# Performance work log

Measured on AMD Instinct MI355X. Metric: run time of the kernel, lower is better.

The kernel has to match this reference:

```python
import jax, jax.numpy as jnp
import numpy as np

B, N = 16, 4096
N_IN, E_OUT = 128, 128          # inpt_dim[1], outp_dim[0]
OUT_N = 128                     # outp_dim[1]
G_DIM, CTXT_DIM = 64, 64
NODE_IN = E_OUT + N_IN          # 256, pre_ln size
CTXT_IN = G_DIM + CTXT_DIM      # 128
HID_F, HID_A = 256, 128
N_HEADS = 4
HEAD_DIM = OUT_N // N_HEADS     # 32
LN_EPS = 1e-5


def _init_w(key, fan_in, fan_out):
    return jax.random.normal(key, (fan_in, fan_out), jnp.float32) / np.float32(np.sqrt(fan_in))


def setup_inputs() -> dict:
    key = jax.random.key(0)
    ks = jax.random.split(key, 10)
    nodes = jax.random.normal(ks[0], (B, N, N_IN), jnp.float32)
    pooled_edges = jax.random.normal(ks[1], (B, N, E_OUT), jnp.float32)
    # variable-length graphs: valid prefix per graph (at least half the nodes)
    lengths = jax.random.randint(ks[2], (B,), N // 2, N + 1)
    mask = jnp.arange(N)[None, :] < lengths[:, None]
    globs = jax.random.normal(ks[3], (B, G_DIM), jnp.float32)
    ctxt = jax.random.normal(ks[4], (B, CTXT_DIM), jnp.float32)
    return {
        "nodes": nodes,
        "pooled_edges": pooled_edges,
        "mask": mask,
        "globs": globs,
        "ctxt": ctxt,
        "ln_g": jnp.ones((NODE_IN,), jnp.float32),
        "ln_b": jnp.zeros((NODE_IN,), jnp.float32),
        "feat_w1": _init_w(ks[5], NODE_IN + CTXT_IN, HID_F),
        "feat_b1": jnp.zeros((HID_F,), jnp.float32),
        "feat_w2": _init_w(ks[6], HID_F, OUT_N),
        "feat_b2": jnp.zeros((OUT_N,), jnp.float32),
        "attn_w1": _init_w(ks[7], NODE_IN + CTXT_IN, HID_A),
        "attn_b1": jnp.zeros((HID_A,), jnp.float32),
        "attn_w2": _init_w(ks[8], HID_A, N_HEADS),
        "attn_b2": jnp.zeros((N_HEADS,), jnp.float32),
    }


def _mlp(x, w1, b1, w2, b2):
    # DenseNetwork: one hidden block with LeakyReLU ("lrlu"), linear output
    h = jax.nn.leaky_relu(x @ w1 + b1)
    return h @ w2 + b2


def reference(nodes, pooled_edges, mask, globs, ctxt, ln_g, ln_b,
              feat_w1, feat_b1, feat_w2, feat_b2,
              attn_w1, attn_b1, attn_w2, attn_b2):
    # nodes = cat([graph.nodes, pooled_edges]) -> pre-LayerNorm
    x = jnp.concatenate([nodes, pooled_edges], axis=-1)           # [B,N,256]
    mu = jnp.mean(x, axis=-1, keepdims=True)
    var = jnp.var(x, axis=-1, keepdims=True)
    x = (x - mu) * jax.lax.rsqrt(var + LN_EPS) * ln_g + ln_b

    # high-level context broadcast to every node
    hl = jnp.concatenate([globs, ctxt], axis=-1)                   # [B,128]
    hl = jnp.broadcast_to(hl[:, None, :], (x.shape[0], x.shape[1], hl.shape[-1]))
    xin = jnp.concatenate([x, hl], axis=-1)                        # [B,N,384]

    # attention net with -inf padding, softmax over node axis (dim=-2)
    logits = _mlp(xin, attn_w1, attn_b1, attn_w2, attn_b2)          # [B,N,H]
    logits = jnp.where(mask[..., None], logits, -jnp.inf)
    w = jax.nn.softmax(logits, axis=1) / np.float32(np.sqrt(OUT_N))
    w = jnp.where(mask[..., None], w, 0.0)

    # feature net with 0 padding + residual (same_size)
    feats = _mlp(xin, feat_w1, feat_b1, feat_w2, feat_b2)           # [B,N,128]
    feats = jnp.where(mask[..., None], feats, 0.0)
    new_nodes = feats + nodes

    # expand per-head weights across head_dim, flatten, weighted node pooling
    w_full = jnp.repeat(w, HEAD_DIM, axis=-1)                       # [B,N,128]
    pooled = jnp.sum(new_nodes * w_full, axis=1)                    # [B,128]
    return (new_nodes, pooled)
```

## Files before the change

### kernel.cpp

```cpp
#include <hip/hip_runtime.h>
#include <stdint.h>

typedef unsigned short u16;
typedef unsigned char  u8;
typedef unsigned int   u32;
typedef __attribute__((ext_vector_type(8))) short bf16x8;
typedef __attribute__((ext_vector_type(4))) float f32x4;

static __device__ __forceinline__ float bf2f(u32 u) {
    union { u32 i; float f; } x; x.i = u << 16; return x.f;
}
static __device__ __forceinline__ u16 f2bf(float f) {
    union { u32 i; float f; } x; x.f = f;
    return (u16)((x.i + 0x7fffu + ((x.i >> 16) & 1u)) >> 16);
}
static __device__ __forceinline__ u32 packbf(float a, float b) {
    return (u32)f2bf(a) | ((u32)f2bf(b) << 16);
}
static __device__ __forceinline__ float ldf(const void* p, int i, int isf32) {
    return isf32 ? ((const float*)p)[i] : bf2f(((const u16*)p)[i]);
}
static __device__ __forceinline__ bool mvalid(const void* mask, int g, int mi32) {
    return mi32 ? (((const int*)mask)[g] != 0) : (((const u8*)mask)[g] != 0);
}

#define NTOT 65536
#define SXLD 260
#define SHLD 132
#define PVLD 136

__global__ __launch_bounds__(256) void k0_prep(
    const void* __restrict__ feat_w1, const void* __restrict__ attn_w1,
    const void* __restrict__ feat_b1, const void* __restrict__ attn_b1,
    const void* __restrict__ feat_w2, const void* __restrict__ attn_w2,
    const void* __restrict__ globs, const void* __restrict__ ctxt,
    const void* __restrict__ ln_g,
    u16* __restrict__ W1t, u16* __restrict__ W2t, u16* __restrict__ aw2t,
    float* __restrict__ hlc)
{
    __shared__ u16 tile[64][66];
    __shared__ float hl[128];
    const int isf32 = (((const u32*)ln_g)[0] == 0x3F800000u);
    const int bid = blockIdx.x;
    const int t = threadIdx.x;

    if (bid < 24) {
        int jt = bid >> 2, kt = bid & 3;
        int j0 = jt * 64, k0 = kt * 64;
        int jj = t & 63, kq = t >> 6;
#pragma unroll
        for (int r = 0; r < 16; r++) {
            int kk = r * 4 + kq;
            int j = j0 + jj;
            float v = (j < 256) ? ldf(feat_w1, (k0 + kk) * 256 + j, isf32)
                                : ldf(attn_w1, (k0 + kk) * 128 + (j - 256), isf32);
            tile[kk][jj] = f2bf(v);
        }
        __syncthreads();
        int kk2 = t & 63, jq = t >> 6;
#pragma unroll
        for (int r = 0; r < 16; r++) {
            int jj2 = r * 4 + jq;
            W1t[(size_t)(j0 + jj2) * 256 + k0 + kk2] = tile[kk2][jj2];
        }
    } else if (bid < 32) {
        int id2 = bid - 24;
        int ct2 = id2 >> 2, kt = id2 & 3;
        int c0 = ct2 * 64, k0 = kt * 64;
        int cc = t & 63, kq = t >> 6;
#pragma unroll
        for (int r = 0; r < 16; r++) {
            int kk = r * 4 + kq;
            tile[kk][cc] = f2bf(ldf(feat_w2, (k0 + kk) * 128 + c0 + cc, isf32));
        }
        __syncthreads();
        int kk2 = t & 63, cq = t >> 6;
#pragma unroll
        for (int r = 0; r < 16; r++) {
            int cc2 = r * 4 + cq;
            W2t[(size_t)(c0 + cc2) * 256 + k0 + kk2] = tile[kk2][cc2];
        }
    } else if (bid == 32) {
#pragma unroll
        for (int i = 0; i < 8; i++) {
            int e = i * 256 + t;
            int n = e >> 7, k = e & 127;
            aw2t[e] = (n < 4) ? f2bf(ldf(attn_w2, k * 4 + n, isf32)) : (u16)0;
        }
    } else {
        int b = bid - 33;
        if (t < 64)       hl[t] = ldf(globs, b * 64 + t, isf32);
        else if (t < 128) hl[t] = ldf(ctxt, b * 64 + (t - 64), isf32);
        __syncthreads();
        {
            float s = ldf(feat_b1, t, isf32);
#pragma unroll 8
            for (int c = 0; c < 128; c++)
                s += hl[c] * ldf(feat_w1, (256 + c) * 256 + t, isf32);
            hlc[b * 384 + t] = s;
        }
        if (t < 128) {
            float s = ldf(attn_b1, t, isf32);
#pragma unroll 8
            for (int c = 0; c < 128; c++)
                s += hl[c] * ldf(attn_w1, (256 + c) * 128 + t, isf32);
            hlc[b * 384 + 256 + t] = s;
        }
    }
}

__global__ __launch_bounds__(256, 3) void k_mega(
    const void* __restrict__ nodes, const void* __restrict__ edges,
    const void* __restrict__ ln_g, const void* __restrict__ ln_b,
    const u16* __restrict__ W1t, const u16* __restrict__ W2t,
    const u16* __restrict__ aw2t, const float* __restrict__ hlc,
    const void* __restrict__ attn_b2, const void* __restrict__ feat_b2,
    const void* __restrict__ mask,
    float* __restrict__ pv, void* __restrict__ outp)
{
    __shared__ __align__(16) u16 sX[64 * SXLD];
    __shared__ __align__(16) u16 sH[64 * SHLD];
    __shared__ float sG[256], sBt[256];
    __shared__ float sL[64][4];
    const int t = threadIdx.x;
    const int g0 = blockIdx.x * 64;
    const int b = g0 >> 12;
    const int isf32 = (((const u32*)ln_g)[0] == 0x3F800000u);
    const int mi32  = (((const u32*)mask)[0] == 1u);

    sG[t]  = ldf(ln_g, t, isf32);
    sBt[t] = ldf(ln_b, t, isf32);
    __syncthreads();

#pragma unroll
    for (int half = 0; half < 2; half++) {
        const int r = half * 32 + (t >> 3), q8 = t & 7;
        u32 pk[16];
#pragma unroll
        for (int j = 0; j < 4; j++) {
            int c = q8 + j * 8;
            if (isf32) {
                const float* src = (c < 16)
                    ? ((const float*)nodes + (size_t)(g0 + r) * 128 + c * 8)
                    : ((const float*)edges + (size_t)(g0 + r) * 128 + (c - 16) * 8);
                float4 v0 = ((const float4*)src)[0];
                float4 v1 = ((const float4*)src)[1];
                pk[4 * j]     = packbf(v0.x, v0.y);
                pk[4 * j + 1] = packbf(v0.z, v0.w);
                pk[4 * j + 2] = packbf(v1.x, v1.y);
                pk[4 * j + 3] = packbf(v1.z, v1.w);
            } else {
                const u16* src = (c < 16)
                    ? ((const u16*)nodes + (size_t)(g0 + r) * 128 + c * 8)
                    : ((const u16*)edges + (size_t)(g0 + r) * 128 + (c - 16) * 8);
                uint4 v = ((const uint4*)src)[0];
                pk[4 * j] = v.x; pk[4 * j + 1] = v.y;
                pk[4 * j + 2] = v.z; pk[4 * j + 3] = v.w;
            }
        }
        float s = 0.f, q = 0.f;
#pragma unroll
        for (int i = 0; i < 16; i++) {
            float lo = bf2f(pk[i] & 0xffffu), hi = bf2f(pk[i] >> 16);
            s += lo + hi; q += lo * lo + hi * hi;
        }
        s += __shfl_xor(s, 1, 64); s += __shfl_xor(s, 2, 64); s += __shfl_xor(s, 4, 64);
        q += __shfl_xor(q, 1, 64); q += __shfl_xor(q, 2, 64); q += __shfl_xor(q, 4, 64);
        float mu = s * (1.f / 256.f);
        float var = q * (1.f / 256.f) - mu * mu;
        float rs = rsqrtf(var + 1e-5f);
#pragma unroll
        for (int j = 0; j < 4; j++) {
            int c = q8 + j * 8;
            u32 ow[4];
#pragma unroll
            for (int k2 = 0; k2 < 4; k2++) {
                int col = c * 8 + k2 * 2;
                u32 w2 = pk[4 * j + k2];
                float y0 = (bf2f(w2 & 0xffffu) - mu) * rs * sG[col]     + sBt[col];
                float y1 = (bf2f(w2 >> 16)     - mu) * rs * sG[col + 1] + sBt[col + 1];
                ow[k2] = packbf(y0, y1);
            }
            *(uint4*)&sX[r * SXLD + c * 8] = make_uint4(ow[0], ow[1], ow[2], ow[3]);
        }
    }
    __syncthreads();

    const int w = t >> 6, l = t & 63;
    const int lr = l & 15, lq = l >> 4;
    const float ab2 = (lr < 4) ? ldf(attn_b2, lr, isf32) : 0.f;
    const float fb2_0 = ldf(feat_b2, w * 32 + lr, isf32);
    const float fb2_1 = ldf(feat_b2, w * 32 + 16 + lr, isf32);

    f32x4 acc2[4][2];
#pragma unroll
    for (int rt = 0; rt < 4; rt++)
#pragma unroll
        for (int ct = 0; ct < 2; ct++) acc2[rt][ct] = (f32x4){0.f, 0.f, 0.f, 0.f};

    const int order[3] = {2, 0, 1};
#pragma unroll
    for (int oi = 0; oi < 3; oi++) {
        const int nt = order[oi];

        float hbv[2];
#pragma unroll
        for (int ct = 0; ct < 2; ct++)
            hbv[ct] = hlc[b * 384 + nt * 128 + w * 32 + ct * 16 + lr];

        f32x4 acc1[4][2];
#pragma unroll
        for (int rt = 0; rt < 4; rt++)
#pragma unroll
            for (int ct = 0; ct < 2; ct++) acc1[rt][ct] = (f32x4){0.f, 0.f, 0.f, 0.f};

        const u16* Wp = W1t + (size_t)(nt * 128 + w * 32 + lr) * 256;
#pragma unroll
        for (int kh = 0; kh < 2; kh++) {
            bf16x8 bW[4][2];
#pragma unroll
            for (int kk = 0; kk < 4; kk++)
#pragma unroll
                for (int ct = 0; ct < 2; ct++)
                    bW[kk][ct] = *(const bf16x8*)(Wp + ct * 16 * 256 + (kh * 4 + kk) * 32 + lq * 8);
#pragma unroll
            for (int kk = 0; kk < 4; kk++) {
                bf16x8 aF[4];
#pragma unroll
                for (int rt = 0; rt < 4; rt++)
                    aF[rt] = *(const bf16x8*)&sX[(rt * 16 + lr) * SXLD + ((kh * 4 + kk) * 4 + lq) * 8];
#pragma unroll
                for (int rt = 0; rt < 4; rt++)
#pragma unroll
                    for (int ct = 0; ct < 2; ct++)
                        acc1[rt][ct] = __builtin_amdgcn_mfma_f32_16x16x32_bf16(aF[rt], bW[kk][ct], acc1[rt][ct], 0, 0, 0);
            }
        }

        __syncthreads();
#pragma unroll
        for (int rt = 0; rt < 4; rt++)
#pragma unroll
            for (int ct = 0; ct < 2; ct++)
#pragma unroll
                for (int reg = 0; reg < 4; reg++) {
                    int row = rt * 16 + lq * 4 + reg;
                    int col = w * 32 + ct * 16 + lr;
                    float hv = acc1[rt][ct][reg] + hbv[ct];
                    hv = (hv >= 0.f) ? hv : 0.01f * hv;
                    sH[row * SHLD + col] = f2bf(hv);
                }
        __syncthreads();

        if (nt == 2) {
            f32x4 accL = (f32x4){0.f, 0.f, 0.f, 0.f};
#pragma unroll
            for (int kk = 0; kk < 4; kk++) {
                bf16x8 aF = *(const bf16x8*)&sH[(w * 16 + lr) * SHLD + (kk * 4 + lq) * 8];
                bf16x8 bF = *(const bf16x8*)(aw2t + lr * 128 + kk * 32 + lq * 8);
                accL = __builtin_amdgcn_mfma_f32_16x16x32_bf16(aF, bF, accL, 0, 0, 0);
            }
            if (lr < 4) {
#pragma unroll
                for (int reg = 0; reg < 4; reg++)
                    sL[w * 16 + lq * 4 + reg][lr] = accL[reg] + ab2;
            }
        } else {
            const u16* W2p = W2t + (size_t)(w * 32 + lr) * 256 + nt * 128;
            bf16x8 bW2[4][2];
#pragma unroll
            for (int kk = 0; kk < 4; kk++)
#pragma unroll
                for (int ct = 0; ct < 2; ct++)
                    bW2[kk][ct] = *(const bf16x8*)(W2p + ct * 16 * 256 + kk * 32 + lq * 8);
#pragma unroll
            for (int kk = 0; kk < 4; kk++) {
                bf16x8 aF[4];
#pragma unroll
                for (int rt = 0; rt < 4; rt++)
                    aF[rt] = *(const bf16x8*)&sH[(rt * 16 + lr) * SHLD + (kk * 4 + lq) * 8];
#pragma unroll
                for (int rt = 0; rt < 4; rt++)
#pragma unroll
                    for (int ct = 0; ct < 2; ct++)
                        acc2[rt][ct] = __builtin_amdgcn_mfma_f32_16x16x32_bf16(aF[rt], bW2[kk][ct], acc2[rt][ct], 0, 0, 0);
            }
        }
    }

    float* pvb = pv + (size_t)blockIdx.x * PVLD;
    if (w == 0) {
        const int row = l;
        const bool vld = mvalid(mask, g0 + row, mi32);
        float lg0 = sL[row][0], lg1 = sL[row][1], lg2 = sL[row][2], lg3 = sL[row][3];
        float x0 = vld ? lg0 : -1e30f;
        float x1 = vld ? lg1 : -1e30f;
        float x2 = vld ? lg2 : -1e30f;
        float x3 = vld ? lg3 : -1e30f;
#pragma unroll
        for (int o = 1; o < 64; o <<= 1) {
            x0 = fmaxf(x0, __shfl_xor(x0, o, 64));
            x1 = fmaxf(x1, __shfl_xor(x1, o, 64));
            x2 = fmaxf(x2, __shfl_xor(x2, o, 64));
            x3 = fmaxf(x3, __shfl_xor(x3, o, 64));
        }
        float e0 = vld ? expf(lg0 - x0) : 0.f;
        float e1 = vld ? expf(lg1 - x1) : 0.f;
        float e2 = vld ? expf(lg2 - x2) : 0.f;
        float e3 = vld ? expf(lg3 - x3) : 0.f;
        sL[row][0] = e0; sL[row][1] = e1; sL[row][2] = e2; sL[row][3] = e3;
        float s0 = e0, s1 = e1, s2 = e2, s3 = e3;
#pragma unroll
        for (int o = 1; o < 64; o <<= 1) {
            s0 += __shfl_xor(s0, o, 64);
            s1 += __shfl_xor(s1, o, 64);
            s2 += __shfl_xor(s2, o, 64);
            s3 += __shfl_xor(s3, o, 64);
        }
        if (l == 0) {
            pvb[128] = s0; pvb[129] = s1; pvb[130] = s2; pvb[131] = s3;
            pvb[132] = x0; pvb[133] = x1; pvb[134] = x2; pvb[135] = x3;
        }
    }
    __syncthreads();

    float pc0 = 0.f, pc1 = 0.f;
#pragma unroll
    for (int rt = 0; rt < 4; rt++)
#pragma unroll
        for (int ct = 0; ct < 2; ct++)
#pragma unroll
            for (int reg = 0; reg < 4; reg++) {
                int row = rt * 16 + lq * 4 + reg;
                int col = w * 32 + ct * 16 + lr;
                int g = g0 + row;
                float v = acc2[rt][ct][reg] + (ct ? fb2_1 : fb2_0);
                v = mvalid(mask, g, mi32) ? v : 0.f;
                v += ldf(nodes, g * 128 + col, isf32);
                size_t idx = (size_t)g * 128 + col;
                if (isf32) ((float*)outp)[idx] = v;
                else       ((u16*)outp)[idx] = f2bf(v);
                float e = sL[row][w];
                if (ct) pc1 += e * v; else pc0 += e * v;
            }
    pc0 += __shfl_xor(pc0, 16, 64); pc0 += __shfl_xor(pc0, 32, 64);
    pc1 += __shfl_xor(pc1, 16, 64); pc1 += __shfl_xor(pc1, 32, 64);
    if (lq == 0) {
        pvb[w * 32 + lr]      = pc0;
        pvb[w * 32 + 16 + lr] = pc1;
    }
}

__global__ __launch_bounds__(256) void k_final(
    const float* __restrict__ pv, const void* __restrict__ ln_g,
    void* __restrict__ outbase)
{
    __shared__ float sm[64][4], ss[64][4], se[64][4];
    __shared__ float sZ[4];
    __shared__ float part[2][128];
    const int b = blockIdx.x;
    const int t = threadIdx.x;
    const int isf32 = (((const u32*)ln_g)[0] == 0x3F800000u);
    const float* pvb = pv + (size_t)b * 64 * PVLD;

#pragma unroll
    for (int i = t; i < 512; i += 256) {
        int rec = i >> 3, j = i & 7;
        float x = pvb[(size_t)rec * PVLD + 128 + j];
        if (j < 4) ss[rec][j] = x;
        else       sm[rec][j - 4] = x;
    }
    __syncthreads();

    {
        const int h = t >> 6, i = t & 63;
        float m = sm[i][h];
#pragma unroll
        for (int o = 1; o < 64; o <<= 1) m = fmaxf(m, __shfl_xor(m, o, 64));
        float e = expf(sm[i][h] - m);
        se[i][h] = e;
        float z = e * ss[i][h];
#pragma unroll
        for (int o = 1; o < 64; o <<= 1) z += __shfl_xor(z, o, 64);
        if (i == 0) sZ[h] = z;
    }
    __syncthreads();

    {
        const int c = t & 127, half = t >> 7;
        const int h = c >> 5;
        float acc = 0.f;
#pragma unroll 8
        for (int j = 0; j < 32; j++) {
            int rec = half * 32 + j;
            acc += se[rec][h] * pvb[(size_t)rec * PVLD + c];
        }
        part[half][c] = acc;
    }
    __syncthreads();
    if (t < 128) {
        float p = (part[0][t] + part[1][t]) * (0.08838834764831845f / sZ[t >> 5]);
        size_t off = (size_t)NTOT * 128 + (size_t)b * 128 + t;
        if (isf32) ((float*)outbase)[off] = p;
        else       ((u16*)outbase)[off] = f2bf(p);
    }
}

extern "C" void kernel_launch(void* const* d_in, const int* in_sizes, int n_in,
                              void* d_out, int out_size, void* d_ws, size_t ws_size,
                              hipStream_t stream)
{
    const void* nodes   = d_in[0];
    const void* edges   = d_in[1];
    const void* mask    = d_in[2];
    const void* globs   = d_in[3];
    const void* ctxt    = d_in[4];
    const void* ln_g    = d_in[5];
    const void* ln_b    = d_in[6];
    const void* feat_w1 = d_in[7];
    const void* feat_b1 = d_in[8];
    const void* feat_w2 = d_in[9];
    const void* feat_b2 = d_in[10];
    const void* attn_w1 = d_in[11];
    const void* attn_b1 = d_in[12];
    const void* attn_w2 = d_in[13];
    const void* attn_b2 = d_in[14];

    char* ws = (char*)d_ws;
    u16*   W1t    = (u16*)ws;   ws += (size_t)384 * 256 * 2;
    u16*   W2t    = (u16*)ws;   ws += (size_t)128 * 256 * 2;
    u16*   aw2t   = (u16*)ws;   ws += (size_t)16 * 128 * 2;
    float* hlc    = (float*)ws; ws += (size_t)16 * 384 * 4;
    float* pv     = (float*)ws; ws += (size_t)1024 * PVLD * 4;

    k0_prep <<<dim3(49),   dim3(256), 0, stream>>>(feat_w1, attn_w1, feat_b1, attn_b1,
                                                   feat_w2, attn_w2, globs, ctxt, ln_g,
                                                   W1t, W2t, aw2t, hlc);
    k_mega  <<<dim3(1024), dim3(256), 0, stream>>>(nodes, edges, ln_g, ln_b, W1t, W2t,
                                                   aw2t, hlc, attn_b2, feat_b2, mask,
                                                   pv, d_out);
    k_final <<<dim3(16),   dim3(256), 0, stream>>>(pv, ln_g, d_out);
}
```

Measured before the change: 220.1 us.

## Distribute softmax across waves and prefetch residual nodes and mask before final GEMM

```diff
diff --git a/kernel.cpp b/kernel.cpp
--- a/kernel.cpp
+++ b/kernel.cpp
@@ -25,9 +25,9 @@
 }
 
 #define NTOT 65536
-#define SXLD 260
-#define SHLD 132
-#define PVLD 136
+#define SXLD 264
+#define SHLD 136
+#define PVLD 144
 
 __global__ __launch_bounds__(256) void k0_prep(
     const void* __restrict__ feat_w1, const void* __restrict__ attn_w1,
@@ -191,12 +191,16 @@
     const float ab2 = (lr < 4) ? ldf(attn_b2, lr, isf32) : 0.f;
     const float fb2_0 = ldf(feat_b2, w * 32 + lr, isf32);
     const float fb2_1 = ldf(feat_b2, w * 32 + 16 + lr, isf32);
+    float* pvb = pv + (size_t)blockIdx.x * PVLD;
 
     f32x4 acc2[4][2];
 #pragma unroll
     for (int rt = 0; rt < 4; rt++)
 #pragma unroll
         for (int ct = 0; ct < 2; ct++) acc2[rt][ct] = (f32x4){0.f, 0.f, 0.f, 0.f};
+
+    float nv[4][2][4];
+    bool  mrow[4][4];
 
     const int order[3] = {2, 0, 1};
 #pragma unroll
@@ -250,6 +254,21 @@
                     hv = (hv >= 0.f) ? hv : 0.01f * hv;
                     sH[row * SHLD + col] = f2bf(hv);
                 }
+
+        if (oi == 1) {
+            const int row = l;
+            const bool vld = mvalid(mask, g0 + row, mi32);
+            float lg = sL[row][w];
+            float x = vld ? lg : -1e30f;
+#pragma unroll
+            for (int o = 1; o < 64; o <<= 1) x = fmaxf(x, __shfl_xor(x, o, 64));
+            float e = vld ? expf(lg - x) : 0.f;
+            sL[row][w] = e;
+            float sgm = e;
+#pragma unroll
+            for (int o = 1; o < 64; o <<= 1) sgm += __shfl_xor(sgm, o, 64);
+            if (l == 0) { pvb[128 + w] = sgm; pvb[132 + w] = x; }
+        }
         __syncthreads();
 
         if (nt == 2) {
@@ -266,6 +285,19 @@
                     sL[w * 16 + lq * 4 + reg][lr] = accL[reg] + ab2;
             }
         } else {
+            if (oi == 2) {
+#pragma unroll
+                for (int rt = 0; rt < 4; rt++)
+#pragma unroll
+                    for (int reg = 0; reg < 4; reg++) {
+                        int row = rt * 16 + lq * 4 + reg;
+                        mrow[rt][reg] = mvalid(mask, g0 + row, mi32);
+#pragma unroll
+                        for (int ct = 0; ct < 2; ct++)
+                            nv[rt][ct][reg] = ldf(nodes,
+                                (g0 + row) * 128 + w * 32 + ct * 16 + lr, isf32);
+                    }
+            }
             const u16* W2p = W2t + (size_t)(w * 32 + lr) * 256 + nt * 128;
             bf16x8 bW2[4][2];
 #pragma unroll
@@ -287,42 +319,6 @@
             }
         }
     }
-
-    float* pvb = pv + (size_t)blockIdx.x * PVLD;
-    if (w == 0) {
-        const int row = l;
-        const bool vld = mvalid(mask, g0 + row, mi32);
-        float lg0 = sL[row][0], lg1 = sL[row][1], lg2 = sL[row][2], lg3 = sL[row][3];
-        float x0 = vld ? lg0 : -1e30f;
-        float x1 = vld ? lg1 : -1e30f;
-        float x2 = vld ? lg2 : -1e30f;
-        float x3 = vld ? lg3 : -1e30f;
-#pragma unroll
-        for (int o = 1; o < 64; o <<= 1) {
-            x0 = fmaxf(x0, __shfl_xor(x0, o, 64));
-            x1 = fmaxf(x1, __shfl_xor(x1, o, 64));
-            x2 = fmaxf(x2, __shfl_xor(x2, o, 64));
-            x3 = fmaxf(x3, __shfl_xor(x3, o, 64));
-        }
-        float e0 = vld ? expf(lg0 - x0) : 0.f;
-        float e1 = vld ? expf(lg1 - x1) : 0.f;
-        float e2 = vld ? expf(lg2 - x2) : 0.f;
-        float e3 = vld ? expf(lg3 - x3) : 0.f;
-        sL[row][0] = e0; sL[row][1] = e1; sL[row][2] = e2; sL[row][3] = e3;
-        float s0 = e0, s1 = e1, s2 = e2, s3 = e3;
-#pragma unroll
-        for (int o = 1; o < 64; o <<= 1) {
-            s0 += __shfl_xor(s0, o, 64);
-            s1 += __shfl_xor(s1, o, 64);
-            s2 += __shfl_xor(s2, o, 64);
-            s3 += __shfl_xor(s3, o, 64);
-        }
-        if (l == 0) {
-            pvb[128] = s0; pvb[129] = s1; pvb[130] = s2; pvb[131] = s3;
-            pvb[132] = x0; pvb[133] = x1; pvb[134] = x2; pvb[135] = x3;
-        }
-    }
-    __syncthreads();
 
     float pc0 = 0.f, pc1 = 0.f;
 #pragma unroll
@@ -335,8 +331,8 @@
                 int col = w * 32 + ct * 16 + lr;
                 int g = g0 + row;
                 float v = acc2[rt][ct][reg] + (ct ? fb2_1 : fb2_0);
-                v = mvalid(mask, g, mi32) ? v : 0.f;
-                v += ldf(nodes, g * 128 + col, isf32);
+                v = mrow[rt][reg] ? v : 0.f;
+                v += nv[rt][ct][reg];
                 size_t idx = (size_t)g * 128 + col;
                 if (isf32) ((float*)outp)[idx] = v;
                 else       ((u16*)outp)[idx] = f2bf(v);
```

Result: faster. 198.0 us (-10.0%).
